# Performance work log

Hardware: AMD Instinct MI355X
Metric: run time of the kernel (lower is better)

The kernel has to match this reference:

```python
import jax, jax.numpy as jnp
import numpy as np

B, L = 1024, 256
D = 64        # neighbor_interaction_feat_dim
TD = 100      # time_encoder.dim
NUM_NODES = 20000


def setup_inputs() -> dict:
    key = jax.random.key(0)
    ks = jax.random.split(key, 12)
    return {
        "src_ids": jax.random.randint(ks[0], (B, L), 0, NUM_NODES),
        "dst_ids": jax.random.randint(ks[1], (B, L), 0, NUM_NODES),
        "src_times": jax.random.uniform(ks[2], (B, L), jnp.float32),
        "dst_times": jax.random.uniform(ks[3], (B, L), jnp.float32),
        "node_times": jax.random.uniform(ks[4], (B,), jnp.float32) + 1.0,
        "num_nodes": NUM_NODES,
        # LTF time encoder: cos(t * w + b)
        "w_time": jax.random.normal(ks[5], (TD,), jnp.float32),
        "b_time": jax.random.normal(ks[6], (TD,), jnp.float32) * 0.1,
        # time_to_scalar: Linear(TD, 1)
        "w_ts": jax.random.normal(ks[7], (TD,), jnp.float32) / np.sqrt(TD),
        "b_ts": jnp.zeros((), jnp.float32),
        # MLP: Linear(1, D) -> ReLU -> Linear(D, D)
        "w1": jax.random.normal(ks[8], (D,), jnp.float32),
        "b1": jax.random.normal(ks[9], (D,), jnp.float32) * 0.1,
        "w2": jax.random.normal(ks[10], (D, D), jnp.float32) / np.sqrt(D),
        "b2": jax.random.normal(ks[11], (D,), jnp.float32) * 0.1,
    }


def _histogram(ids, num_nodes):
    # per-row count of each node id, with id==0 treated as padding (count 0)
    b = ids.shape[0]
    mask = (ids != 0).astype(jnp.float32)
    hist = jnp.zeros((b, num_nodes), jnp.float32)
    return hist.at[jnp.arange(b)[:, None], ids].add(mask)


def _time_weight(time_diff, w_time, b_time, w_ts, b_ts):
    # LTF: cos(t*w + b) -> Linear(TD,1) -> sigmoid, all fused elementwise+dot
    feat = jnp.cos(time_diff[..., None] * w_time + b_time)  # (B,L,TD)
    return jax.nn.sigmoid(feat @ w_ts + b_ts)               # (B,L)


def _mlp_sum(weighted_counts, w1, b1, w2, b2):
    # weighted_counts: (B,L,2) scalar counts -> Linear(1,D) -> ReLU -> Linear(D,D), sum over axis 2
    h = jax.nn.relu(weighted_counts[..., None] * w1 + b1)   # (B,L,2,D)
    return (h @ w2 + b2).sum(axis=2)                        # (B,L,D)


def reference(src_ids, dst_ids, src_times, dst_times, node_times, num_nodes,
              w_time, b_time, w_ts, b_ts, w1, b1, w2, b2):
    hist_src = _histogram(src_ids, num_nodes)  # (B,N)
    hist_dst = _histogram(dst_ids, num_nodes)

    c_ss = jnp.take_along_axis(hist_src, src_ids, axis=1)
    c_sd = jnp.take_along_axis(hist_dst, src_ids, axis=1)
    c_ds = jnp.take_along_axis(hist_src, dst_ids, axis=1)
    c_dd = jnp.take_along_axis(hist_dst, dst_ids, axis=1)

    src_counts = jnp.stack([c_ss, c_sd], axis=2)  # (B,L,2)
    dst_counts = jnp.stack([c_ds, c_dd], axis=2)

    src_w = _time_weight(node_times[:, None] - src_times, w_time, b_time, w_ts, b_ts)
    dst_w = _time_weight(node_times[:, None] - dst_times, w_time, b_time, w_ts, b_ts)

    src_features = _mlp_sum(src_counts * src_w[..., None], w1, b1, w2, b2)
    dst_features = _mlp_sum(dst_counts * dst_w[..., None], w1, b1, w2, b2)
    return src_features, dst_features
```

## Files before the change

### kernel.cpp

```cpp
#include <hip/hip_runtime.h>

#define BB 1024
#define LL 256
#define DD 64
#define TDIM 100
#define NNODES 20000
#define HWORDS ((NNODES + 1) / 2)

typedef _Float16 half8_t __attribute__((ext_vector_type(8)));
typedef float f32x4 __attribute__((ext_vector_type(4)));

__global__ __launch_bounds__(256, 2) void tni_kernel(
    const int* __restrict__ src_ids, const int* __restrict__ dst_ids,
    const float* __restrict__ src_tm, const float* __restrict__ dst_tm,
    const float* __restrict__ node_tm,
    const float* __restrict__ w_time, const float* __restrict__ b_time,
    const float* __restrict__ w_ts, const float* __restrict__ b_ts,
    const float* __restrict__ w1, const float* __restrict__ b1,
    const float* __restrict__ w2, const float* __restrict__ b2,
    float* __restrict__ out)
{
    __shared__ unsigned int uS[10240];
    __shared__ float wrv[TDIM], brv[TDIM], wtsv[TDIM];
    __shared__ float w1v[DD], b1v[DD];

    unsigned int* hist = uS;
    half8_t* W2v = (half8_t*)uS;
    half8_t* Gv  = (half8_t*)(uS + 2048);

    const int t    = threadIdx.x;
    const int b    = blockIdx.x >> 1;
    const int side = blockIdx.x & 1;

    const int   sid   = src_ids[b*LL + t];
    const int   did   = dst_ids[b*LL + t];
    const float my_tm = side ? dst_tm[b*LL + t] : src_tm[b*LL + t];

    float w2r[16];
    #pragma unroll
    for (int i = 0; i < 16; ++i) w2r[i] = w2[t + 256*i];

    if (t < TDIM) {
        const float inv2pi = 0.15915494309189535f;
        wrv[t]  = w_time[t] * inv2pi;
        brv[t]  = b_time[t] * inv2pi;
        wtsv[t] = w_ts[t];
    }
    if (t < DD) {
        w1v[t] = w1[t];
        b1v[t] = b1[t];
    }

    const int sw = sid >> 1, ssh = (sid & 1) * 16;
    const int dw = did >> 1, dsh = (did & 1) * 16;
    const int myw  = side ? dw  : sw;
    const int mysh = side ? dsh : ssh;
    const int my_id = side ? did : sid;

    hist[sw] = 0; hist[dw] = 0;
    __syncthreads();
    if (sid) atomicAdd(&hist[sw], 1u << ssh);
    __syncthreads();
    unsigned c1 = (hist[myw] >> mysh) & 0xffffu;
    __syncthreads();
    hist[sw] = 0; hist[dw] = 0;
    __syncthreads();
    if (did) atomicAdd(&hist[dw], 1u << dsh);
    __syncthreads();
    unsigned c2 = (hist[myw] >> mysh) & 0xffffu;
    if (my_id == 0) { c1 = 0; c2 = 0; }
    __syncthreads();

    float td = node_tm[b] - my_tm;
    float z  = b_ts[0];
    #pragma unroll 4
    for (int k = 0; k < TDIM; ++k) {
        float r = fmaf(td, wrv[k], brv[k]);
        r -= floorf(r);
        z = fmaf(__builtin_amdgcn_cosf(r), wtsv[k], z);
    }
    float ee  = __builtin_amdgcn_exp2f(-1.44269504f * z);
    float wgt = __builtin_amdgcn_rcpf(1.0f + ee);
    float c1w = (float)c1 * wgt;
    float c2w = (float)c2 * wgt;

    {
        _Float16* w2s = (_Float16*)W2v;
        #pragma unroll
        for (int i = 0; i < 16; ++i) {
            int idx = t + 256*i;
            int e = idx >> 6, d = idx & 63;
            int chunk = (e >> 3) ^ (d & 7);
            w2s[d*64 + (chunk << 3) + (e & 7)] = (_Float16)w2r[i];
        }
    }

    #pragma unroll
    for (int c = 0; c < 8; ++c) {
        half8_t h;
        #pragma unroll
        for (int j = 0; j < 8; ++j) {
            float w1e = w1v[c*8 + j], b1e = b1v[c*8 + j];
            float g = fmaxf(fmaf(c1w, w1e, b1e), 0.f)
                    + fmaxf(fmaf(c2w, w1e, b1e), 0.f);
            h[j] = (_Float16)g;
        }
        Gv[t*8 + (c ^ (t & 7))] = h;
    }
    __syncthreads();

    const int w    = t >> 6;
    const int l    = t & 63;
    const int quad = l >> 4;
    const int lr   = l & 15;

    f32x4 acc[4][4];
    #pragma unroll
    for (int mt = 0; mt < 4; ++mt)
        #pragma unroll
        for (int nt = 0; nt < 4; ++nt) {
            f32x4 zz = {0.f, 0.f, 0.f, 0.f};
            acc[mt][nt] = zz;
        }

    #pragma unroll
    for (int s = 0; s < 2; ++s) {
        const int c = s*4 + quad;
        half8_t bfr[4], afr[4];
        #pragma unroll
        for (int nt = 0; nt < 4; ++nt) {
            int n = nt*16 + lr;
            bfr[nt] = W2v[n*8 + (c ^ (n & 7))];
        }
        #pragma unroll
        for (int mt = 0; mt < 4; ++mt) {
            int row = w*64 + mt*16 + lr;
            afr[mt] = Gv[row*8 + (c ^ (row & 7))];
        }
        #pragma unroll
        for (int mt = 0; mt < 4; ++mt)
            #pragma unroll
            for (int nt = 0; nt < 4; ++nt)
                acc[mt][nt] = __builtin_amdgcn_mfma_f32_16x16x32_f16(
                    afr[mt], bfr[nt], acc[mt][nt], 0, 0, 0);
    }

    float b2v[4];
    #pragma unroll
    for (int nt = 0; nt < 4; ++nt)
        b2v[nt] = 2.f * b2[nt*16 + lr];

    const int obase = side * (BB*LL*DD) + b * (LL*DD);
    #pragma unroll
    for (int mt = 0; mt < 4; ++mt) {
        #pragma unroll
        for (int r = 0; r < 4; ++r) {
            int pos = w*64 + mt*16 + quad*4 + r;
            #pragma unroll
            for (int nt = 0; nt < 4; ++nt) {
                out[obase + pos*DD + nt*16 + lr] = acc[mt][nt][r] + b2v[nt];
            }
        }
    }
}

extern "C" void kernel_launch(void* const* d_in, const int* in_sizes, int n_in,
                              void* d_out, int out_size, void* d_ws, size_t ws_size,
                              hipStream_t stream) {
    const int* src_ids = (const int*)d_in[0];
    const int* dst_ids = (const int*)d_in[1];
    const float* src_tm  = (const float*)d_in[2];
    const float* dst_tm  = (const float*)d_in[3];
    const float* node_tm = (const float*)d_in[4];
    const float* w_time = (const float*)d_in[6];
    const float* b_time = (const float*)d_in[7];
    const float* w_ts   = (const float*)d_in[8];
    const float* b_ts   = (const float*)d_in[9];
    const float* w1     = (const float*)d_in[10];
    const float* b1     = (const float*)d_in[11];
    const float* w2     = (const float*)d_in[12];
    const float* b2     = (const float*)d_in[13];
    float* out = (float*)d_out;

    tni_kernel<<<dim3(BB*2), dim3(256), 0, stream>>>(
        src_ids, dst_ids, src_tm, dst_tm, node_tm,
        w_time, b_time, w_ts, b_ts, w1, b1, w2, b2, out);
}
```

Baseline: 169.0 us.

## Process both src and dst sides in one block to share histogram work

Each block now handles one batch row for both sides, not one side per block. It builds the two histograms once and produces src and dst counts, time weights and MLP outputs together. This removes the duplicated histogram construction, id loads and W2 staging that the old two-blocks-per-row split performed, and halves the grid. In exchange each block uses more registers (two accumulator sets) and more shared memory, which may reduce occupancy, and there are fewer blocks to fill the GPU.

```diff
diff --git a/kernel.cpp b/kernel.cpp
--- a/kernel.cpp
+++ b/kernel.cpp
@@ -4,8 +4,6 @@
 #define LL 256
 #define DD 64
 #define TDIM 100
-#define NNODES 20000
-#define HWORDS ((NNODES + 1) / 2)
 
 typedef _Float16 half8_t __attribute__((ext_vector_type(8)));
 typedef float f32x4 __attribute__((ext_vector_type(4)));
@@ -21,20 +19,22 @@
     float* __restrict__ out)
 {
     __shared__ unsigned int uS[10240];
+    __shared__ half8_t G1[LL*8];
     __shared__ float wrv[TDIM], brv[TDIM], wtsv[TDIM];
     __shared__ float w1v[DD], b1v[DD];
 
     unsigned int* hist = uS;
     half8_t* W2v = (half8_t*)uS;
-    half8_t* Gv  = (half8_t*)(uS + 2048);
-
-    const int t    = threadIdx.x;
-    const int b    = blockIdx.x >> 1;
-    const int side = blockIdx.x & 1;
-
-    const int   sid   = src_ids[b*LL + t];
-    const int   did   = dst_ids[b*LL + t];
-    const float my_tm = side ? dst_tm[b*LL + t] : src_tm[b*LL + t];
+    half8_t* G0  = (half8_t*)(uS + 2048);
+
+    const int t = threadIdx.x;
+    const int b = blockIdx.x;
+
+    const int   sid  = src_ids[b*LL + t];
+    const int   did  = dst_ids[b*LL + t];
+    const float s_tm = src_tm[b*LL + t];
+    const float d_tm = dst_tm[b*LL + t];
+    const float ntm  = node_tm[b];
 
     float w2r[16];
     #pragma unroll
@@ -46,43 +46,27 @@
         brv[t]  = b_time[t] * inv2pi;
         wtsv[t] = w_ts[t];
     }
-    if (t < DD) {
-        w1v[t] = w1[t];
-        b1v[t] = b1[t];
-    }
+    if (t < DD) { w1v[t] = w1[t]; b1v[t] = b1[t]; }
 
     const int sw = sid >> 1, ssh = (sid & 1) * 16;
     const int dw = did >> 1, dsh = (did & 1) * 16;
-    const int myw  = side ? dw  : sw;
-    const int mysh = side ? dsh : ssh;
-    const int my_id = side ? did : sid;
 
     hist[sw] = 0; hist[dw] = 0;
     __syncthreads();
     if (sid) atomicAdd(&hist[sw], 1u << ssh);
     __syncthreads();
-    unsigned c1 = (hist[myw] >> mysh) & 0xffffu;
+    unsigned c_ss = (hist[sw] >> ssh) & 0xffffu;
+    unsigned c_ds = (hist[dw] >> dsh) & 0xffffu;
     __syncthreads();
     hist[sw] = 0; hist[dw] = 0;
     __syncthreads();
     if (did) atomicAdd(&hist[dw], 1u << dsh);
     __syncthreads();
-    unsigned c2 = (hist[myw] >> mysh) & 0xffffu;
-    if (my_id == 0) { c1 = 0; c2 = 0; }
-    __syncthreads();
-
-    float td = node_tm[b] - my_tm;
-    float z  = b_ts[0];
-    #pragma unroll 4
-    for (int k = 0; k < TDIM; ++k) {
-        float r = fmaf(td, wrv[k], brv[k]);
-        r -= floorf(r);
-        z = fmaf(__builtin_amdgcn_cosf(r), wtsv[k], z);
-    }
-    float ee  = __builtin_amdgcn_exp2f(-1.44269504f * z);
-    float wgt = __builtin_amdgcn_rcpf(1.0f + ee);
-    float c1w = (float)c1 * wgt;
-    float c2w = (float)c2 * wgt;
+    unsigned c_sd = (hist[sw] >> ssh) & 0xffffu;
+    unsigned c_dd = (hist[dw] >> dsh) & 0xffffu;
+    if (sid == 0) { c_ss = 0; c_sd = 0; }
+    if (did == 0) { c_ds = 0; c_dd = 0; }
+    __syncthreads();
 
     {
         _Float16* w2s = (_Float16*)W2v;
@@ -95,38 +79,61 @@
         }
     }
 
+    const float td_s = ntm - s_tm;
+    const float td_d = ntm - d_tm;
+    float zs = b_ts[0], zd = zs;
+    #pragma unroll 4
+    for (int k = 0; k < TDIM; ++k) {
+        float wk = wrv[k], bk = brv[k], ck = wtsv[k];
+        float rs = fmaf(td_s, wk, bk); rs -= floorf(rs);
+        zs = fmaf(__builtin_amdgcn_cosf(rs), ck, zs);
+        float rd = fmaf(td_d, wk, bk); rd -= floorf(rd);
+        zd = fmaf(__builtin_amdgcn_cosf(rd), ck, zd);
+    }
+    const float wgt_s = __builtin_amdgcn_rcpf(
+        1.0f + __builtin_amdgcn_exp2f(-1.44269504f * zs));
+    const float wgt_d = __builtin_amdgcn_rcpf(
+        1.0f + __builtin_amdgcn_exp2f(-1.44269504f * zd));
+
+    const float c1w0 = (float)c_ss * wgt_s, c2w0 = (float)c_sd * wgt_s;
+    const float c1w1 = (float)c_ds * wgt_d, c2w1 = (float)c_dd * wgt_d;
+
     #pragma unroll
     for (int c = 0; c < 8; ++c) {
-        half8_t h;
+        half8_t h0, h1;
         #pragma unroll
         for (int j = 0; j < 8; ++j) {
             float w1e = w1v[c*8 + j], b1e = b1v[c*8 + j];
-            float g = fmaxf(fmaf(c1w, w1e, b1e), 0.f)
-                    + fmaxf(fmaf(c2w, w1e, b1e), 0.f);
-            h[j] = (_Float16)g;
-        }
-        Gv[t*8 + (c ^ (t & 7))] = h;
-    }
-    __syncthreads();
-
-    const int w    = t >> 6;
+            h0[j] = (_Float16)(fmaxf(fmaf(c1w0, w1e, b1e), 0.f)
+                             + fmaxf(fmaf(c2w0, w1e, b1e), 0.f));
+            h1[j] = (_Float16)(fmaxf(fmaf(c1w1, w1e, b1e), 0.f)
+                             + fmaxf(fmaf(c2w1, w1e, b1e), 0.f));
+        }
+        int gi = t*8 + (c ^ (t & 7));
+        G0[gi] = h0;
+        G1[gi] = h1;
+    }
+    __syncthreads();
+
+    const int wv   = t >> 6;
     const int l    = t & 63;
     const int quad = l >> 4;
     const int lr   = l & 15;
 
-    f32x4 acc[4][4];
+    f32x4 acc0[4][4], acc1[4][4];
     #pragma unroll
     for (int mt = 0; mt < 4; ++mt)
         #pragma unroll
         for (int nt = 0; nt < 4; ++nt) {
             f32x4 zz = {0.f, 0.f, 0.f, 0.f};
-            acc[mt][nt] = zz;
+            acc0[mt][nt] = zz;
+            acc1[mt][nt] = zz;
         }
 
     #pragma unroll
     for (int s = 0; s < 2; ++s) {
         const int c = s*4 + quad;
-        half8_t bfr[4], afr[4];
+        half8_t bfr[4], afr0[4], afr1[4];
         #pragma unroll
         for (int nt = 0; nt < 4; ++nt) {
             int n = nt*16 + lr;
@@ -134,31 +141,40 @@
         }
         #pragma unroll
         for (int mt = 0; mt < 4; ++mt) {
-            int row = w*64 + mt*16 + lr;
-            afr[mt] = Gv[row*8 + (c ^ (row & 7))];
+            int row = wv*64 + mt*16 + lr;
+            int gi  = row*8 + (c ^ (row & 7));
+            afr0[mt] = G0[gi];
+            afr1[mt] = G1[gi];
         }
         #pragma unroll
         for (int mt = 0; mt < 4; ++mt)
             #pragma unroll
-            for (int nt = 0; nt < 4; ++nt)
-                acc[mt][nt] = __builtin_amdgcn_mfma_f32_16x16x32_f16(
-                    afr[mt], bfr[nt], acc[mt][nt], 0, 0, 0);
+            for (int nt = 0; nt < 4; ++nt) {
+                acc0[mt][nt] = __builtin_amdgcn_mfma_f32_16x16x32_f16(
+                    afr0[mt], bfr[nt], acc0[mt][nt], 0, 0, 0);
+                acc1[mt][nt] = __builtin_amdgcn_mfma_f32_16x16x32_f16(
+                    afr1[mt], bfr[nt], acc1[mt][nt], 0, 0, 0);
+            }
     }
 
     float b2v[4];
     #pragma unroll
-    for (int nt = 0; nt < 4; ++nt)
-        b2v[nt] = 2.f * b2[nt*16 + lr];
-
-    const int obase = side * (BB*LL*DD) + b * (LL*DD);
+    for (int nt = 0; nt < 4; ++nt) b2v[nt] = 2.f * b2[nt*16 + lr];
+
+    const int obase0 = b * (LL*DD);
+    const int obase1 = (BB*LL*DD) + b * (LL*DD);
     #pragma unroll
     for (int mt = 0; mt < 4; ++mt) {
         #pragma unroll
         for (int r = 0; r < 4; ++r) {
-            int pos = w*64 + mt*16 + quad*4 + r;
+            int po = (wv*64 + mt*16 + quad*4 + r) * DD;
             #pragma unroll
             for (int nt = 0; nt < 4; ++nt) {
-                out[obase + pos*DD + nt*16 + lr] = acc[mt][nt][r] + b2v[nt];
+                out[obase0 + po + nt*16 + lr] = acc0[mt][nt][r] + b2v[nt];
+            }
+            #pragma unroll
+            for (int nt = 0; nt < 4; ++nt) {
+                out[obase1 + po + nt*16 + lr] = acc1[mt][nt][r] + b2v[nt];
             }
         }
     }
@@ -182,7 +198,7 @@
     const float* b2     = (const float*)d_in[13];
     float* out = (float*)d_out;
 
-    tni_kernel<<<dim3(BB*2), dim3(256), 0, stream>>>(
+    tni_kernel<<<dim3(BB), dim3(256), 0, stream>>>(
         src_ids, dst_ids, src_tm, dst_tm, node_tm,
         w_time, b_time, w_ts, b_ts, w1, b1, w2, b2, out);
 }
```

Result: no change. 169.3 us (+0.2%).
